# Performance work log

Hardware: AMD Instinct MI355X
Metric: run time of the kernel (lower is better)

The kernel has to match this reference:

```python
import jax, jax.numpy as jnp
import numpy as np
from jax import lax

H_IMG, W_IMG = 512, 640
PX, PY = 600.0, 600.0
U0, V0 = 320.0, 256.0
BORDER = 5
CH = H_IMG - 2 * BORDER  # cropped height
CW = W_IMG - 2 * BORDER  # cropped width
N = CH * CW
# 7-tap derivative filter (as in ImageGradients)
F = jnp.array([-112.0, -913.0, -2047.0, 0.0, 2047.0, 913.0, 112.0], dtype=jnp.float32) / 8418.0


def setup_inputs() -> dict:
    key = jax.random.key(0)
    k1, k2, k3, k4 = jax.random.split(key, 4)
    B = 64
    Is = jax.random.normal(k1, (B, H_IMG, W_IMG), dtype=jnp.float32)
    Ids = jax.random.normal(k2, (B, H_IMG, W_IMG), dtype=jnp.float32)
    Zinv = jax.random.uniform(k3, (B, H_IMG, W_IMG), dtype=jnp.float32) + 0.1  # positive inverse depth
    mu = jax.random.uniform(k4, (B,), dtype=jnp.float32)
    return {"Is": Is, "Ids": Ids, "Zinv": Zinv, "mu": mu}


def _image_gradients(x):
    # x: (B, H, W). Cross-correlation with 7-tap filter (matches torch conv2d).
    b = BORDER
    xi = x[:, None, b:-b, b - 3:-(b - 3)]       # (B,1,CH,CW+6)
    yi = x[:, None, b - 3:-(b - 3), b:-b]       # (B,1,CH+6,CW)
    kx = F.reshape(1, 1, 1, 7)
    ky = F.reshape(1, 1, 7, 1)
    Ix = lax.conv_general_dilated(xi, kx, (1, 1), 'VALID')[:, 0]  # (B,CH,CW)
    Iy = lax.conv_general_dilated(yi, ky, (1, 1), 'VALID')[:, 0]  # (B,CH,CW)
    return Ix, Iy


def _dvs_forward(Is, Ids, Zinv, mu):
    b = BORDER
    B = Is.shape[0]
    # crop + flatten
    Zv = Zinv[:, b:-b, b:-b].reshape(B, N)
    Isv = Is[:, b:-b, b:-b].reshape(B, N)
    Idsv = Ids[:, b:-b, b:-b].reshape(B, N)
    Idx, Idy = _image_gradients(Ids)
    Ixv = Idx.reshape(B, N) * PX
    Iyv = Idy.reshape(B, N) * PY
    # normalized image coordinates per pixel (flattened row-major)
    xs = (jnp.arange(b, W_IMG - b, dtype=jnp.float32) - U0) / PX  # (CW,)
    ys = (jnp.arange(b, H_IMG - b, dtype=jnp.float32) - V0) / PY  # (CH,)
    xsf = jnp.tile(xs, CH)                 # (N,)
    ysf = jnp.repeat(ys, CW)               # (N,)
    xsys = xsf * ysf
    # interaction matrix columns -> (B, N, 6)
    Lsd = jnp.stack([
        Ixv * Zv,
        Iyv * Zv,
        -(xsf * Ixv + ysf * Iyv) * Zv,
        -Ixv * xsys - (1.0 + ysf ** 2) * Iyv,
        (1.0 + xsf ** 2) * Ixv + Iyv * xsys,
        Iyv * xsf - Ixv * ysf,
    ], axis=-1)
    # Gauss-Newton Hessian (B,6,6) via tall-skinny reduction
    Hsd = jnp.einsum('bni,bnj->bij', Lsd, Lsd)
    diags = jnp.diagonal(Hsd, axis1=-2, axis2=-1)        # (B,6)
    diagHsd = jnp.eye(6, dtype=Hsd.dtype) * diags[:, None, :]
    Hinv = jnp.linalg.inv(mu[:, None, None] * diagHsd + Hsd)
    e = Isv - Idsv                                        # (B,N)
    g = jnp.einsum('bni,bn->bi', Lsd, e)                  # Lsd^T e
    vc = -jnp.einsum('bij,bj->bi', Hinv, g)               # (B,6)
    return vc


def reference(Is, Ids, Zinv, mu):
    return _dvs_forward(Is, Ids, Zinv, mu)
```

## Files before the change

kernel.cpp:

```cpp
#include <hip/hip_runtime.h>
#include <math.h>


namespace {
constexpr int HI = 512, WI = 640, BRD = 5;
constexpr int RPT = 4;
constexpr int TILES = 128;
constexpr int TG = TILES / 4;
constexpr int SEGS = 3;
constexpr int BLK_PER_B = SEGS * TG;
constexpr float PXc = 600.0f, PYc = 600.0f, U0c = 320.0f, V0c = 256.0f;
constexpr float G1 = 2047.0f / 8418.0f * 600.0f;
constexpr float G2 = 913.0f  / 8418.0f * 600.0f;
constexpr float G3 = 112.0f  / 8418.0f * 600.0f;
}

__device__ __forceinline__ float elem(const float4 v, int q) {
    return q == 0 ? v.x : (q == 1 ? v.y : (q == 2 ? v.z : v.w));
}

__global__ __launch_bounds__(256) void dvs_partial(
    const float* __restrict__ Is, const float* __restrict__ Ids,
    const float* __restrict__ Zinv, float* __restrict__ ws)
{
    const int tid  = threadIdx.x;
    const int lane = tid & 63;
    const int wv   = tid >> 6;
    const int b   = blockIdx.x / BLK_PER_B;
    const int rem = blockIdx.x - b * BLK_PER_B;
    const int seg = rem / TG;
    const int tg  = rem - seg * TG;
    const int tile = tg * 4 + wv;
    const int r0 = BRD + tile * RPT;

    const int base = (seg == 0) ? 0   : ((seg == 1) ? 200 : 384);
    const int lo   = (seg == 0) ? 5   : ((seg == 1) ? 252 : 452);
    const int hi   = (seg == 0) ? 252 : ((seg == 1) ? 452 : 635);
    const int c0 = base + (lane << 2);

    const size_t ofs = (size_t)b * (HI * WI);
    const float* __restrict__ Ib = Is   + ofs;
    const float* __restrict__ Db = Ids  + ofs;
    const float* __restrict__ Zb = Zinv + ofs;

    float msk[4], xk[4], opx[4];
#pragma unroll
    for (int q = 0; q < 4; ++q) {
        const int c = c0 + q;
        msk[q] = (c >= lo && c < hi) ? 1.0f : 0.0f;
        xk[q]  = ((float)c - U0c) * (1.0f / PXc);
        opx[q] = 1.0f + xk[q] * xk[q];
    }

    float4 win[10];
#pragma unroll
    for (int j = 0; j < 10; ++j) {
        const int rr = min(r0 - 3 + j, HI - 1);
        win[j] = *(const float4*)(Db + rr * WI + c0);
    }
    float4 isv[4], zvv[4];
#pragma unroll
    for (int k = 0; k < RPT; ++k) {
        const int rr = min(r0 + k, HI - 1);
        isv[k] = *(const float4*)(Ib + rr * WI + c0);
        zvv[k] = *(const float4*)(Zb + rr * WI + c0);
    }

    float acc[27];
#pragma unroll
    for (int t = 0; t < 27; ++t) acc[t] = 0.0f;

    const int lm = (lane + 63) & 63, lp = (lane + 1) & 63;

#pragma unroll
    for (int k = 0; k < RPT; ++k) {
        const int rc = r0 + k;
        const float rmk = (rc < HI - BRD) ? 1.0f : 0.0f;
        const float4 a0 = win[k], a1 = win[k + 1], a2 = win[k + 2],
                     ct = win[k + 3], a4 = win[k + 4], a5 = win[k + 5],
                     a6 = win[k + 6];
        const float hl1 = __shfl(ct.w, lm);
        const float hl2 = __shfl(ct.z, lm);
        const float hl3 = __shfl(ct.y, lm);
        const float hr1 = __shfl(ct.x, lp);
        const float hr2 = __shfl(ct.y, lp);
        const float hr3 = __shfl(ct.z, lp);
        const float h[10] = {hl3, hl2, hl1, ct.x, ct.y, ct.z, ct.w,
                             hr1, hr2, hr3};
        const float yv  = ((float)rc - V0c) * (1.0f / PYc);
        const float opy = 1.0f + yv * yv;
        const float4 isV = isv[k], zV = zvv[k];
#pragma unroll
        for (int q = 0; q < 4; ++q) {
            const float m  = msk[q] * rmk;
            const float Ix = (G1 * (h[q + 4] - h[q + 2]) +
                              G2 * (h[q + 5] - h[q + 1]) +
                              G3 * (h[q + 6] - h[q])) * m;
            const float Iy = (G1 * (elem(a4, q) - elem(a2, q)) +
                              G2 * (elem(a5, q) - elem(a1, q)) +
                              G3 * (elem(a6, q) - elem(a0, q))) * m;
            const float Z  = elem(zV, q);
            const float e  = elem(isV, q) - elem(ct, q);
            const float x  = xk[q], xy = x * yv;
            float L[6];
            L[0] = Ix * Z;
            L[1] = Iy * Z;
            L[2] = -(x * Ix + yv * Iy) * Z;
            L[3] = -Ix * xy - opy * Iy;
            L[4] = opx[q] * Ix + Iy * xy;
            L[5] = Iy * x - Ix * yv;
            int t = 0;
#pragma unroll
            for (int i = 0; i < 6; ++i)
#pragma unroll
                for (int j = i; j < 6; ++j)
                    acc[t++] += L[i] * L[j];
#pragma unroll
            for (int i = 0; i < 6; ++i) acc[21 + i] += L[i] * e;
        }
    }

#pragma unroll
    for (int t = 0; t < 27; ++t) {
        float v = acc[t];
        v += __shfl_xor(v, 1);  v += __shfl_xor(v, 2);  v += __shfl_xor(v, 4);
        v += __shfl_xor(v, 8);  v += __shfl_xor(v, 16); v += __shfl_xor(v, 32);
        acc[t] = v;
    }
    float outv = acc[0];
#pragma unroll
    for (int t = 1; t < 27; ++t) if (lane == t) outv = acc[t];

    __shared__ float red[4][28];
    if (lane < 27) red[wv][lane] = outv;
    __syncthreads();
    if (tid < 27) {
        float s = red[0][tid] + red[1][tid] + red[2][tid] + red[3][tid];
        ws[(size_t)blockIdx.x * 27 + tid] = s;
    }
}

__global__ __launch_bounds__(128) void dvs_solve(
    const float* __restrict__ ws, const float* __restrict__ mu,
    float* __restrict__ out)
{
    const int b = blockIdx.x;
    __shared__ float sd[27][BLK_PER_B + 1];
    for (int i = threadIdx.x; i < BLK_PER_B * 27; i += 128) {
        const int s = i / 27, k = i - s * 27;
        sd[k][s] = ws[((size_t)b * BLK_PER_B + s) * 27 + k];
    }
    __syncthreads();
    __shared__ double hsum[27];
    if (threadIdx.x < 27) {
        double t = 0.0;
        for (int s = 0; s < BLK_PER_B; ++s) t += (double)sd[threadIdx.x][s];
        hsum[threadIdx.x] = t;
    }
    __syncthreads();
    if (threadIdx.x == 0) {
        double A[6][7];
        int k = 0;
        for (int i = 0; i < 6; ++i)
            for (int j = i; j < 6; ++j) { A[i][j] = hsum[k]; A[j][i] = hsum[k]; ++k; }
        const double dm = 1.0 + (double)mu[b];
        for (int i = 0; i < 6; ++i) { A[i][i] *= dm; A[i][6] = hsum[21 + i]; }
        for (int col = 0; col < 6; ++col) {
            int p = col; double best = fabs(A[col][col]);
            for (int r = col + 1; r < 6; ++r) {
                const double vv = fabs(A[r][col]);
                if (vv > best) { best = vv; p = r; }
            }
            if (p != col)
                for (int cc = col; cc < 7; ++cc) {
                    const double t = A[col][cc]; A[col][cc] = A[p][cc]; A[p][cc] = t;
                }
            const double inv = 1.0 / A[col][col];
            for (int r = col + 1; r < 6; ++r) {
                const double f = A[r][col] * inv;
                for (int cc = col + 1; cc < 7; ++cc) A[r][cc] -= f * A[col][cc];
            }
        }
        double xs[6];
        for (int i = 5; i >= 0; --i) {
            double s = A[i][6];
            for (int j = i + 1; j < 6; ++j) s -= A[i][j] * xs[j];
            xs[i] = s / A[i][i];
        }
        for (int i = 0; i < 6; ++i) out[b * 6 + i] = (float)(-xs[i]);
    }
}

extern "C" void kernel_launch(void* const* d_in, const int* in_sizes, int n_in,
                              void* d_out, int out_size, void* d_ws, size_t ws_size,
                              hipStream_t stream)
{
    const float* Is   = (const float*)d_in[0];
    const float* Ids  = (const float*)d_in[1];
    const float* Zinv = (const float*)d_in[2];
    const float* mu   = (const float*)d_in[3];
    const int B = in_sizes[3];
    float* out = (float*)d_out;
    float* ws  = (float*)d_ws;

    dvs_partial<<<B * BLK_PER_B, 256, 0, stream>>>(Is, Ids, Zinv, ws);
    dvs_solve<<<B, 128, 0, stream>>>(ws, mu, out);
}
```

Measured before the change: 70.30 us.

## Stage Ids row window in shared memory to share halo rows across waves

Each block now cooperatively loads a 22-row by 264-column tile of Ids, including vertical and horizontal halos, into LDS. Waves then read their 10-row windows and left/right neighbours from LDS instead of each wave issuing redundant global loads and cross-lane shuffles. This cuts duplicated global traffic for the overlapping vertical halo, which was reloaded 2.5x per wave. In exchange it adds about 23 KB of LDS per block, a block-wide barrier and extra LDS reads, which may lower occupancy.

```diff
diff --git a/kernel.cpp b/kernel.cpp
--- a/kernel.cpp
+++ b/kernel.cpp
@@ -5,10 +5,13 @@
 namespace {
 constexpr int HI = 512, WI = 640, BRD = 5;
 constexpr int RPT = 4;
-constexpr int TILES = 128;
-constexpr int TG = TILES / 4;
+constexpr int WVS = 4;
+constexpr int RB  = RPT * WVS;
+constexpr int TG  = 32;
 constexpr int SEGS = 3;
 constexpr int BLK_PER_B = SEGS * TG;
+constexpr int TW = 264;
+constexpr int TR = RB + 6;
 constexpr float PXc = 600.0f, PYc = 600.0f, U0c = 320.0f, V0c = 256.0f;
 constexpr float G1 = 2047.0f / 8418.0f * 600.0f;
 constexpr float G2 = 913.0f  / 8418.0f * 600.0f;
@@ -30,18 +33,33 @@
     const int rem = blockIdx.x - b * BLK_PER_B;
     const int seg = rem / TG;
     const int tg  = rem - seg * TG;
-    const int tile = tg * 4 + wv;
-    const int r0 = BRD + tile * RPT;
-
-    const int base = (seg == 0) ? 0   : ((seg == 1) ? 200 : 384);
-    const int lo   = (seg == 0) ? 5   : ((seg == 1) ? 252 : 452);
-    const int hi   = (seg == 0) ? 252 : ((seg == 1) ? 452 : 635);
-    const int c0 = base + (lane << 2);
+
+    const int sbase = (seg == 0) ? -4  : ((seg == 1) ? 196 : 380);
+    const int base  = sbase + 4;
+    const int lo    = (seg == 0) ? 5   : ((seg == 1) ? 252 : 452);
+    const int hi    = (seg == 0) ? 252 : ((seg == 1) ? 452 : 635);
+    const int blk_r0 = BRD + tg * RB;
 
     const size_t ofs = (size_t)b * (HI * WI);
     const float* __restrict__ Ib = Is   + ofs;
     const float* __restrict__ Db = Ids  + ofs;
     const float* __restrict__ Zb = Zinv + ofs;
+
+    __shared__ float tile[TR][TW];
+    __shared__ float red[WVS][28];
+
+    for (int i = tid; i < TR * (TW / 4); i += 256) {
+        const int rr = i / (TW / 4);
+        const int c4 = i - rr * (TW / 4);
+        const int gr = min(blk_r0 - 3 + rr, HI - 1);
+        int gc = sbase + c4 * 4;
+        gc = max(0, min(gc, WI - 4));
+        *(float4*)&tile[rr][c4 * 4] = *(const float4*)(Db + gr * WI + gc);
+    }
+
+    const int r0 = blk_r0 + wv * RPT;
+    const int c0 = base + (lane << 2);
+    const int lc = 4 + (lane << 2);
 
     float msk[4], xk[4], opx[4];
 #pragma unroll
@@ -52,13 +70,7 @@
         opx[q] = 1.0f + xk[q] * xk[q];
     }
 
-    float4 win[10];
-#pragma unroll
-    for (int j = 0; j < 10; ++j) {
-        const int rr = min(r0 - 3 + j, HI - 1);
-        win[j] = *(const float4*)(Db + rr * WI + c0);
-    }
-    float4 isv[4], zvv[4];
+    float4 isv[RPT], zvv[RPT];
 #pragma unroll
     for (int k = 0; k < RPT; ++k) {
         const int rr = min(r0 + k, HI - 1);
@@ -66,11 +78,16 @@
         zvv[k] = *(const float4*)(Zb + rr * WI + c0);
     }
 
+    __syncthreads();
+
+    float4 win[10];
+#pragma unroll
+    for (int j = 0; j < 10; ++j)
+        win[j] = *(const float4*)&tile[wv * RPT + j][lc];
+
     float acc[27];
 #pragma unroll
     for (int t = 0; t < 27; ++t) acc[t] = 0.0f;
-
-    const int lm = (lane + 63) & 63, lp = (lane + 1) & 63;
 
 #pragma unroll
     for (int k = 0; k < RPT; ++k) {
@@ -79,14 +96,10 @@
         const float4 a0 = win[k], a1 = win[k + 1], a2 = win[k + 2],
                      ct = win[k + 3], a4 = win[k + 4], a5 = win[k + 5],
                      a6 = win[k + 6];
-        const float hl1 = __shfl(ct.w, lm);
-        const float hl2 = __shfl(ct.z, lm);
-        const float hl3 = __shfl(ct.y, lm);
-        const float hr1 = __shfl(ct.x, lp);
-        const float hr2 = __shfl(ct.y, lp);
-        const float hr3 = __shfl(ct.z, lp);
-        const float h[10] = {hl3, hl2, hl1, ct.x, ct.y, ct.z, ct.w,
-                             hr1, hr2, hr3};
+        const float4 lw = *(const float4*)&tile[wv * RPT + k + 3][lc - 4];
+        const float4 rw = *(const float4*)&tile[wv * RPT + k + 3][lc + 4];
+        const float h[10] = {lw.y, lw.z, lw.w, ct.x, ct.y, ct.z, ct.w,
+                             rw.x, rw.y, rw.z};
         const float yv  = ((float)rc - V0c) * (1.0f / PYc);
         const float opy = 1.0f + yv * yv;
         const float4 isV = isv[k], zV = zvv[k];
@@ -131,7 +144,6 @@
 #pragma unroll
     for (int t = 1; t < 27; ++t) if (lane == t) outv = acc[t];
 
-    __shared__ float red[4][28];
     if (lane < 27) red[wv][lane] = outv;
     __syncthreads();
     if (tid < 27) {
```

New measurement: 92.15 us. 1.31x slower.

## Double rows per wave, stream Is/Zinv rows, and refactor L math into FMAs

Applied to the files above, without the earlier changes.

Each wave now handles 8 rows instead of 4, so the 6-row vertical halo of the derivative window is shared across more output rows and fewer blocks and partial sums are written. Is and Zinv rows are loaded one row ahead through a two-entry buffer rather than all up front, which keeps register pressure down; an occupancy hint of 4 blocks is also added. The interaction-matrix terms are rewritten with fmaf and shared products. The cost is fewer blocks in flight and more work per wave, which may reduce latency hiding.

```diff
diff --git a/kernel.cpp b/kernel.cpp
--- a/kernel.cpp
+++ b/kernel.cpp
@@ -4,11 +4,12 @@
 
 namespace {
 constexpr int HI = 512, WI = 640, BRD = 5;
-constexpr int RPT = 4;
-constexpr int TILES = 128;
-constexpr int TG = TILES / 4;
+constexpr int RPT = 8;
+constexpr int TILES = 64;
+constexpr int WVS = 4;
+constexpr int BPS = TILES / WVS;
 constexpr int SEGS = 3;
-constexpr int BLK_PER_B = SEGS * TG;
+constexpr int BLK_PER_B = SEGS * BPS;
 constexpr float PXc = 600.0f, PYc = 600.0f, U0c = 320.0f, V0c = 256.0f;
 constexpr float G1 = 2047.0f / 8418.0f * 600.0f;
 constexpr float G2 = 913.0f  / 8418.0f * 600.0f;
@@ -19,7 +20,7 @@
     return q == 0 ? v.x : (q == 1 ? v.y : (q == 2 ? v.z : v.w));
 }
 
-__global__ __launch_bounds__(256) void dvs_partial(
+__global__ __launch_bounds__(256, 4) void dvs_partial(
     const float* __restrict__ Is, const float* __restrict__ Ids,
     const float* __restrict__ Zinv, float* __restrict__ ws)
 {
@@ -28,9 +29,9 @@
     const int wv   = tid >> 6;
     const int b   = blockIdx.x / BLK_PER_B;
     const int rem = blockIdx.x - b * BLK_PER_B;
-    const int seg = rem / TG;
-    const int tg  = rem - seg * TG;
-    const int tile = tg * 4 + wv;
+    const int seg = rem / BPS;
+    const int bg  = rem - seg * BPS;
+    const int tile = bg * WVS + wv;
     const int r0 = BRD + tile * RPT;
 
     const int base = (seg == 0) ? 0   : ((seg == 1) ? 200 : 384);
@@ -43,37 +44,41 @@
     const float* __restrict__ Db = Ids  + ofs;
     const float* __restrict__ Zb = Zinv + ofs;
 
-    float msk[4], xk[4], opx[4];
+    float msk[4], xk[4];
 #pragma unroll
     for (int q = 0; q < 4; ++q) {
         const int c = c0 + q;
         msk[q] = (c >= lo && c < hi) ? 1.0f : 0.0f;
         xk[q]  = ((float)c - U0c) * (1.0f / PXc);
-        opx[q] = 1.0f + xk[q] * xk[q];
-    }
-
-    float4 win[10];
-#pragma unroll
-    for (int j = 0; j < 10; ++j) {
+    }
+
+    float4 win[14];
+#pragma unroll
+    for (int j = 0; j < 14; ++j) {
         const int rr = min(r0 - 3 + j, HI - 1);
         win[j] = *(const float4*)(Db + rr * WI + c0);
     }
-    float4 isv[4], zvv[4];
+    float4 isb[2], zvb[2];
+    {
+        const int rr = min(r0, HI - 1);
+        isb[0] = *(const float4*)(Ib + rr * WI + c0);
+        zvb[0] = *(const float4*)(Zb + rr * WI + c0);
+    }
+    isb[1] = isb[0]; zvb[1] = zvb[0];
+
+    float acc[27];
+#pragma unroll
+    for (int t = 0; t < 27; ++t) acc[t] = 0.0f;
+
+    const int lm = (lane + 63) & 63, lp = (lane + 1) & 63;
+
 #pragma unroll
     for (int k = 0; k < RPT; ++k) {
-        const int rr = min(r0 + k, HI - 1);
-        isv[k] = *(const float4*)(Ib + rr * WI + c0);
-        zvv[k] = *(const float4*)(Zb + rr * WI + c0);
-    }
-
-    float acc[27];
-#pragma unroll
-    for (int t = 0; t < 27; ++t) acc[t] = 0.0f;
-
-    const int lm = (lane + 63) & 63, lp = (lane + 1) & 63;
-
-#pragma unroll
-    for (int k = 0; k < RPT; ++k) {
+        if (k < RPT - 1) {
+            const int rr = min(r0 + k + 1, HI - 1);
+            isb[(k + 1) & 1] = *(const float4*)(Ib + rr * WI + c0);
+            zvb[(k + 1) & 1] = *(const float4*)(Zb + rr * WI + c0);
+        }
         const int rc = r0 + k;
         const float rmk = (rc < HI - BRD) ? 1.0f : 0.0f;
         const float4 a0 = win[k], a1 = win[k + 1], a2 = win[k + 2],
@@ -88,26 +93,26 @@
         const float h[10] = {hl3, hl2, hl1, ct.x, ct.y, ct.z, ct.w,
                              hr1, hr2, hr3};
         const float yv  = ((float)rc - V0c) * (1.0f / PYc);
-        const float opy = 1.0f + yv * yv;
-        const float4 isV = isv[k], zV = zvv[k];
+        const float4 isV = isb[k & 1], zV = zvb[k & 1];
 #pragma unroll
         for (int q = 0; q < 4; ++q) {
             const float m  = msk[q] * rmk;
-            const float Ix = (G1 * (h[q + 4] - h[q + 2]) +
-                              G2 * (h[q + 5] - h[q + 1]) +
-                              G3 * (h[q + 6] - h[q])) * m;
-            const float Iy = (G1 * (elem(a4, q) - elem(a2, q)) +
-                              G2 * (elem(a5, q) - elem(a1, q)) +
-                              G3 * (elem(a6, q) - elem(a0, q))) * m;
+            const float Ix = fmaf(G3, h[q + 6] - h[q],
+                              fmaf(G2, h[q + 5] - h[q + 1],
+                                   G1 * (h[q + 4] - h[q + 2]))) * m;
+            const float Iy = fmaf(G3, elem(a6, q) - elem(a0, q),
+                              fmaf(G2, elem(a5, q) - elem(a1, q),
+                                   G1 * (elem(a4, q) - elem(a2, q)))) * m;
             const float Z  = elem(zV, q);
             const float e  = elem(isV, q) - elem(ct, q);
             const float x  = xk[q], xy = x * yv;
+            const float tt = x * Ix, uu = yv * Iy;
             float L[6];
             L[0] = Ix * Z;
             L[1] = Iy * Z;
-            L[2] = -(x * Ix + yv * Iy) * Z;
-            L[3] = -Ix * xy - opy * Iy;
-            L[4] = opx[q] * Ix + Iy * xy;
+            L[2] = -(tt + uu) * Z;
+            L[3] = -(fmaf(yv, uu, Iy) + Ix * xy);
+            L[4] = fmaf(x, tt, Ix) + Iy * xy;
             L[5] = Iy * x - Ix * yv;
             int t = 0;
 #pragma unroll
@@ -131,7 +136,7 @@
 #pragma unroll
     for (int t = 1; t < 27; ++t) if (lane == t) outv = acc[t];
 
-    __shared__ float red[4][28];
+    __shared__ float red[WVS][28];
     if (lane < 27) red[wv][lane] = outv;
     __syncthreads();
     if (tid < 27) {
```

New measurement: 238.2 us. 3.39x slower.
